# Optimization experiments

Hardware: AMD Instinct MI355X
Metric: run time of the kernel (lower is better)

The kernel has to match this reference:

```python
import jax, jax.numpy as jnp
import numpy as np

C_IN = 128
D_K = 256
D_V = 256
N_HEAD = 8
H = 192
W = 192
REGION = 3
TEMPER = int(np.sqrt(D_K))  # int(sqrt(d_k)) per the torch module


def setup_inputs() -> dict:
    key = jax.random.key(0)
    k1, k2, k3, k4 = jax.random.split(key, 4)
    scale = 1.0 / np.sqrt(C_IN).astype(np.float32)
    x = jax.random.normal(k1, (1, C_IN, H, W), dtype=jnp.float32)
    wq = jax.random.normal(k2, (D_K, C_IN), dtype=jnp.float32) * scale
    wk = jax.random.normal(k3, (D_K, C_IN), dtype=jnp.float32) * scale
    wv = jax.random.normal(k4, (D_V, C_IN), dtype=jnp.float32) * scale
    return {"x": x, "wq": wq, "wk": wk, "wv": wv}


def _stretch(t):
    # Equivalent of the fixed Conv3d 'stretch' trick: for each (i, j) in the
    # 3x3 region, channel 3*i+j holds the input shifted by (i-1, j-1), zero-padded.
    # t: [b, d, H, W] -> [b, 9, d, H, W]
    b, d, h, w = t.shape
    tp = jnp.pad(t, ((0, 0), (0, 0), (1, 1), (1, 1)))
    return jnp.stack(
        [tp[:, :, i:i + h, j:j + w] for i in range(REGION) for j in range(REGION)],
        axis=1,
    )


def reference(x, wq, wk, wv):
    b = x.shape[0]  # must be 1 (module's broadcast only works for batch 1)
    dkh = D_K // N_HEAD
    dvh = D_V // N_HEAD
    r2 = REGION * REGION
    # 1x1 conv projections == channel matmuls
    q = jnp.einsum('oc,bchw->bohw', wq, x)
    k = jnp.einsum('oc,bchw->bohw', wk, x)
    v = jnp.einsum('oc,bchw->bohw', wv, x)
    Q = _stretch(q)  # [b, 9, d_k, H, W]
    K = _stretch(k)
    V = _stretch(v)  # [b, 9, d_v, H, W]
    # elementwise QK, per-head channel sum, scale, softmax over the 9 region slots
    qk = (Q * K).reshape(b, r2, N_HEAD, dkh, H, W)
    scores = jax.nn.softmax(qk.sum(axis=3) / TEMPER, axis=1)  # [b, 9, n_head, H, W]
    # dropout is identity in eval mode (att_drop disabled for the reference)
    Vh = V.reshape(b, r2, N_HEAD, dvh, H, W)
    out = (scores[:, :, :, None] * Vh).sum(axis=1).reshape(b, D_V, H, W)
    return out
```

## Files before the change

kernel.cpp:

```cpp
#include <hip/hip_runtime.h>

#define HW_   36864
#define WI    192
#define HT    192
#define CIN   128
#define DK    256
#define NH    8
#define DKH   32

using short4_ = __attribute__((ext_vector_type(4))) short;
using short8  = __attribute__((ext_vector_type(8))) short;
using float4_ = __attribute__((ext_vector_type(4))) float;

static __device__ __forceinline__ float b2f(unsigned short u) {
    union { unsigned int i; float f; } x; x.i = ((unsigned int)u) << 16; return x.f;
}
static __device__ __forceinline__ unsigned short f2b(float f) {
    union { float f; unsigned int i; } x; x.f = f;
    unsigned int r = x.i + 0x7FFFu + ((x.i >> 16) & 1u);
    return (unsigned short)(r >> 16);
}

__global__ __launch_bounds__(256) void conv_kernel(
    const float* __restrict__ x,
    const float* __restrict__ wq,
    const float* __restrict__ wk,
    const float* __restrict__ wv,
    unsigned short* __restrict__ xt,
    unsigned short* __restrict__ wqkv)
{
    const int t = threadIdx.x;
    if (blockIdx.x >= 576) {
        int id = (blockIdx.x - 576) * 256 + t;
        int h   = id / 12288;
        int rem = id - h * 12288;
        int r   = rem >> 7;
        int c   = rem & 127;
        const float* __restrict__ s = (r < 32) ? wq : ((r < 64) ? wk : wv);
        wqkv[id] = f2b(s[(h * 32 + (r & 31)) * 128 + c]);
        return;
    }
    __shared__ unsigned short tile[64][136];
    const int px0 = blockIdx.x * 64;
    for (int i = 0; i < 32; ++i) {
        int id = i * 256 + t;
        int c = id >> 6, p = id & 63;
        tile[p][c] = f2b(x[c * HW_ + px0 + p]);
    }
    __syncthreads();
    for (int i = 0; i < 4; ++i) {
        int id = i * 256 + t;
        int row = id >> 4, c8 = id & 15;
        *(short8*)&xt[(px0 + row) * 128 + c8 * 8] =
            *(const short8*)&tile[row][c8 * 8];
    }
}

__global__ __launch_bounds__(256) void projmm_kernel(
    const unsigned short* __restrict__ xt,
    const unsigned short* __restrict__ wqkv,
    unsigned short* __restrict__ vbuf,
    float* __restrict__ sbuf)
{
    const int head = blockIdx.x;
    const int px0  = blockIdx.y * 128;
    const int t    = threadIdx.x;
    const int lane = t & 63, wave = t >> 6;
    const int col  = lane & 15, quad = lane >> 4;

    const unsigned short* __restrict__ Ag = wqkv + head * 96 * 128;
    const unsigned short* __restrict__ Bg = xt + (size_t)px0 * 128;

    short8 bfrag[2][4];
    #pragma unroll
    for (int nt = 0; nt < 2; ++nt)
        #pragma unroll
        for (int kt = 0; kt < 4; ++kt) {
            int n = wave * 32 + nt * 16 + col;
            bfrag[nt][kt] = *(const short8*)&Bg[n * 128 + kt * 32 + quad * 8];
        }

    float4_ acc[6][2];
    #pragma unroll
    for (int mt = 0; mt < 6; ++mt)
        #pragma unroll
        for (int nt = 0; nt < 2; ++nt)
            acc[mt][nt] = (float4_){0.f, 0.f, 0.f, 0.f};

    #pragma unroll
    for (int mt = 0; mt < 6; ++mt) {
        #pragma unroll
        for (int kt = 0; kt < 4; ++kt) {
            short8 a = *(const short8*)&Ag[(mt * 16 + col) * 128 + kt * 32 + quad * 8];
            acc[mt][0] = __builtin_amdgcn_mfma_f32_16x16x32_bf16(a, bfrag[0][kt], acc[mt][0], 0, 0, 0);
            acc[mt][1] = __builtin_amdgcn_mfma_f32_16x16x32_bf16(a, bfrag[1][kt], acc[mt][1], 0, 0, 0);
        }
    }

    #pragma unroll
    for (int nt = 0; nt < 2; ++nt) {
        int px = px0 + wave * 32 + nt * 16 + col;
        float s = 0.f;
        #pragma unroll
        for (int reg = 0; reg < 4; ++reg)
            s += acc[0][nt][reg] * acc[2][nt][reg]
               + acc[1][nt][reg] * acc[3][nt][reg];
        s += __shfl_xor(s, 16, 64);
        s += __shfl_xor(s, 32, 64);
        if (quad == 0) sbuf[head * HW_ + px] = s;
        unsigned short* vp = vbuf + ((size_t)head * HW_ + px) * 32;
        short4_ v0, v1;
        #pragma unroll
        for (int reg = 0; reg < 4; ++reg) {
            v0[reg] = (short)f2b(acc[4][nt][reg]);
            v1[reg] = (short)f2b(acc[5][nt][reg]);
        }
        *(short4_*)&vp[quad * 4]      = v0;
        *(short4_*)&vp[16 + quad * 4] = v1;
    }
}

__global__ __launch_bounds__(256) void attn_kernel(
    const unsigned short* __restrict__ vbuf,
    const float* __restrict__ sbuf,
    float* __restrict__ out)
{
    __shared__ float tr[32][65];
    const int b    = blockIdx.x;
    const int tile = b % 576;
    const int head = b / 576;
    const int t    = threadIdx.x;
    const int pxl  = t >> 2;
    const int cg   = t & 3;
    const int px   = tile * 64 + pxl;
    const int y    = px / WI;
    const int xx   = px - y * WI;

    const float* __restrict__ Sh = sbuf + head * HW_;

    float w[9];
    int   np[9];
    float m = -1e30f;
    #pragma unroll
    for (int r = 0; r < 9; ++r) {
        int dy = r / 3 - 1, dx = r % 3 - 1;
        int ny = y + dy, nx = xx + dx;
        bool inb = (ny >= 0) && (ny < HT) && (nx >= 0) && (nx < WI);
        int idx = inb ? (ny * WI + nx) : px;
        np[r] = idx;
        float val = inb ? (Sh[idx] * 0.0625f) : 0.0f;
        w[r] = val;
        m = fmaxf(m, val);
    }
    float wsum = 0.f;
    #pragma unroll
    for (int r = 0; r < 9; ++r) {
        float e = __expf(w[r] - m);
        w[r] = e;
        wsum += e;
    }
    float inv = 1.0f / wsum;
    #pragma unroll
    for (int r = 0; r < 9; ++r) {
        int dy = r / 3 - 1, dx = r % 3 - 1;
        int ny = y + dy, nx = xx + dx;
        bool inb = (ny >= 0) && (ny < HT) && (nx >= 0) && (nx < WI);
        w[r] = inb ? (w[r] * inv) : 0.0f;
    }

    const unsigned short* __restrict__ vb = vbuf + (size_t)head * HW_ * 32;
    float acc[8] = {0.f, 0.f, 0.f, 0.f, 0.f, 0.f, 0.f, 0.f};
    #pragma unroll
    for (int r = 0; r < 9; ++r) {
        short8 v8 = *(const short8*)&vb[np[r] * 32 + cg * 8];
        #pragma unroll
        for (int j = 0; j < 8; ++j)
            acc[j] = fmaf(w[r], b2f((unsigned short)v8[j]), acc[j]);
    }
    #pragma unroll
    for (int j = 0; j < 8; ++j)
        tr[cg * 8 + j][pxl] = acc[j];
    __syncthreads();

    const int ch = t >> 3, c8 = t & 7;
    const int px0 = tile * 64;
    const size_t obase = (size_t)(head * DKH + ch) * HW_ + px0 + c8 * 8;
    float4_ o0, o1;
    #pragma unroll
    for (int j = 0; j < 4; ++j) {
        o0[j] = tr[ch][c8 * 8 + j];
        o1[j] = tr[ch][c8 * 8 + 4 + j];
    }
    float* o = out + obase;
    *(float4_*)&o[0] = o0;
    *(float4_*)&o[4] = o1;
}

extern "C" void kernel_launch(void* const* d_in, const int* in_sizes, int n_in,
                              void* d_out, int out_size, void* d_ws, size_t ws_size,
                              hipStream_t stream) {
    const float* x  = (const float*)d_in[0];
    const float* wq = (const float*)d_in[1];
    const float* wk = (const float*)d_in[2];
    const float* wv = (const float*)d_in[3];

    char* ws = (char*)d_ws;
    unsigned short* wqkv = (unsigned short*)ws;
    unsigned short* xt   = (unsigned short*)(ws + 196608);
    unsigned short* vbuf = (unsigned short*)(ws + 9633792);
    float*          sbuf = (float*)(ws + 28508160);

    conv_kernel<<<960, 256, 0, stream>>>(x, wq, wk, wv, xt, wqkv);
    projmm_kernel<<<dim3(8, 288), 256, 0, stream>>>(xt, wqkv, vbuf, sbuf);
    attn_kernel<<<4608, 256, 0, stream>>>(vbuf, sbuf, (float*)d_out);
}
```

Before: 134.5 us.

## Fuse input transpose into projection kernel and loop over heads per pixel tile

```diff
diff --git a/kernel.cpp b/kernel.cpp
--- a/kernel.cpp
+++ b/kernel.cpp
@@ -21,90 +21,80 @@
     return (unsigned short)(r >> 16);
 }
 
-__global__ __launch_bounds__(256) void conv_kernel(
-    const float* __restrict__ x,
+__global__ __launch_bounds__(256) void convw_kernel(
     const float* __restrict__ wq,
     const float* __restrict__ wk,
     const float* __restrict__ wv,
-    unsigned short* __restrict__ xt,
     unsigned short* __restrict__ wqkv)
 {
-    const int t = threadIdx.x;
-    if (blockIdx.x >= 576) {
-        int id = (blockIdx.x - 576) * 256 + t;
-        int h   = id / 12288;
-        int rem = id - h * 12288;
-        int r   = rem >> 7;
-        int c   = rem & 127;
-        const float* __restrict__ s = (r < 32) ? wq : ((r < 64) ? wk : wv);
-        wqkv[id] = f2b(s[(h * 32 + (r & 31)) * 128 + c]);
-        return;
-    }
-    __shared__ unsigned short tile[64][136];
-    const int px0 = blockIdx.x * 64;
-    for (int i = 0; i < 32; ++i) {
-        int id = i * 256 + t;
-        int c = id >> 6, p = id & 63;
-        tile[p][c] = f2b(x[c * HW_ + px0 + p]);
-    }
-    __syncthreads();
-    for (int i = 0; i < 4; ++i) {
-        int id = i * 256 + t;
-        int row = id >> 4, c8 = id & 15;
-        *(short8*)&xt[(px0 + row) * 128 + c8 * 8] =
-            *(const short8*)&tile[row][c8 * 8];
-    }
-}
-
-__global__ __launch_bounds__(256) void projmm_kernel(
-    const unsigned short* __restrict__ xt,
+    int id = blockIdx.x * 256 + threadIdx.x;
+    int h   = id / 12288;
+    int rem = id - h * 12288;
+    int r   = rem >> 7;
+    int c   = rem & 127;
+    const float* __restrict__ s = (r < 32) ? wq : ((r < 64) ? wk : wv);
+    wqkv[id] = f2b(s[(h * 32 + (r & 31)) * 128 + c]);
+}
+
+__global__ __launch_bounds__(256) void projfused2_kernel(
+    const float* __restrict__ x,
     const unsigned short* __restrict__ wqkv,
     unsigned short* __restrict__ vbuf,
     float* __restrict__ sbuf)
 {
-    const int head = blockIdx.x;
-    const int px0  = blockIdx.y * 128;
-    const int t    = threadIdx.x;
+    __shared__ unsigned short Sh[96 * 136];
+    const int px0 = blockIdx.x * 64;
+    const int t   = threadIdx.x;
     const int lane = t & 63, wave = t >> 6;
     const int col  = lane & 15, quad = lane >> 4;
 
-    const unsigned short* __restrict__ Ag = wqkv + head * 96 * 128;
-    const unsigned short* __restrict__ Bg = xt + (size_t)px0 * 128;
-
-    short8 bfrag[2][4];
-    #pragma unroll
-    for (int nt = 0; nt < 2; ++nt)
-        #pragma unroll
-        for (int kt = 0; kt < 4; ++kt) {
-            int n = wave * 32 + nt * 16 + col;
-            bfrag[nt][kt] = *(const short8*)&Bg[n * 128 + kt * 32 + quad * 8];
+    #pragma unroll 4
+    for (int i = 0; i < 32; ++i) {
+        int id = i * 256 + t;
+        int c = id >> 6, p = id & 63;
+        Sh[p * 136 + c] = f2b(x[c * HW_ + px0 + p]);
+    }
+    __syncthreads();
+
+    short8 bfrag[4];
+    {
+        int n = wave * 16 + col;
+        #pragma unroll
+        for (int kt = 0; kt < 4; ++kt)
+            bfrag[kt] = *(const short8*)&Sh[n * 136 + kt * 32 + quad * 8];
+    }
+
+    for (int head = 0; head < 8; ++head) {
+        __syncthreads();
+        const unsigned short* __restrict__ Ag = wqkv + head * 96 * 128;
+        #pragma unroll
+        for (int i = 0; i < 6; ++i) {
+            int id = i * 256 + t;
+            int row = id >> 4, c8 = id & 15;
+            *(short8*)&Sh[row * 136 + c8 * 8] = *(const short8*)&Ag[row * 128 + c8 * 8];
         }
-
-    float4_ acc[6][2];
-    #pragma unroll
-    for (int mt = 0; mt < 6; ++mt)
-        #pragma unroll
-        for (int nt = 0; nt < 2; ++nt)
-            acc[mt][nt] = (float4_){0.f, 0.f, 0.f, 0.f};
-
-    #pragma unroll
-    for (int mt = 0; mt < 6; ++mt) {
-        #pragma unroll
-        for (int kt = 0; kt < 4; ++kt) {
-            short8 a = *(const short8*)&Ag[(mt * 16 + col) * 128 + kt * 32 + quad * 8];
-            acc[mt][0] = __builtin_amdgcn_mfma_f32_16x16x32_bf16(a, bfrag[0][kt], acc[mt][0], 0, 0, 0);
-            acc[mt][1] = __builtin_amdgcn_mfma_f32_16x16x32_bf16(a, bfrag[1][kt], acc[mt][1], 0, 0, 0);
+        __syncthreads();
+
+        float4_ acc[6];
+        #pragma unroll
+        for (int mt = 0; mt < 6; ++mt)
+            acc[mt] = (float4_){0.f, 0.f, 0.f, 0.f};
+
+        #pragma unroll
+        for (int mt = 0; mt < 6; ++mt) {
+            #pragma unroll
+            for (int kt = 0; kt < 4; ++kt) {
+                short8 a = *(const short8*)&Sh[(mt * 16 + col) * 136 + kt * 32 + quad * 8];
+                acc[mt] = __builtin_amdgcn_mfma_f32_16x16x32_bf16(a, bfrag[kt], acc[mt], 0, 0, 0);
+            }
         }
-    }
-
-    #pragma unroll
-    for (int nt = 0; nt < 2; ++nt) {
-        int px = px0 + wave * 32 + nt * 16 + col;
+
+        int px = px0 + wave * 16 + col;
         float s = 0.f;
         #pragma unroll
         for (int reg = 0; reg < 4; ++reg)
-            s += acc[0][nt][reg] * acc[2][nt][reg]
-               + acc[1][nt][reg] * acc[3][nt][reg];
+            s += acc[0][reg] * acc[2][reg]
+               + acc[1][reg] * acc[3][reg];
         s += __shfl_xor(s, 16, 64);
         s += __shfl_xor(s, 32, 64);
         if (quad == 0) sbuf[head * HW_ + px] = s;
@@ -112,8 +102,8 @@
         short4_ v0, v1;
         #pragma unroll
         for (int reg = 0; reg < 4; ++reg) {
-            v0[reg] = (short)f2b(acc[4][nt][reg]);
-            v1[reg] = (short)f2b(acc[5][nt][reg]);
+            v0[reg] = (short)f2b(acc[4][reg]);
+            v1[reg] = (short)f2b(acc[5][reg]);
         }
         *(short4_*)&vp[quad * 4]      = v0;
         *(short4_*)&vp[16 + quad * 4] = v1;
@@ -206,11 +196,10 @@
 
     char* ws = (char*)d_ws;
     unsigned short* wqkv = (unsigned short*)ws;
-    unsigned short* xt   = (unsigned short*)(ws + 196608);
-    unsigned short* vbuf = (unsigned short*)(ws + 9633792);
-    float*          sbuf = (float*)(ws + 28508160);
-
-    conv_kernel<<<960, 256, 0, stream>>>(x, wq, wk, wv, xt, wqkv);
-    projmm_kernel<<<dim3(8, 288), 256, 0, stream>>>(xt, wqkv, vbuf, sbuf);
+    unsigned short* vbuf = (unsigned short*)(ws + 196608);
+    float*          sbuf = (float*)(ws + 19071104);
+
+    convw_kernel<<<384, 256, 0, stream>>>(wq, wk, wv, wqkv);
+    projfused2_kernel<<<576, 256, 0, stream>>>(x, wqkv, vbuf, sbuf);
     attn_kernel<<<4608, 256, 0, stream>>>(vbuf, sbuf, (float*)d_out);
 }
```

Measured after the change: 119.0 us. 11.5% less time.
